# Kernel tuning notes

Measured on AMD Instinct MI355X. Metric: run time of the kernel, lower is better.

Reference implementation:

```python
import jax, jax.numpy as jnp
import numpy as np


def setup_inputs() -> dict:
    key = jax.random.key(0)
    k1, k2 = jax.random.split(key)
    N, M, D = 16384, 16384, 3
    target_pc = jax.random.normal(k1, (N, D), dtype=jnp.float32)
    output_pc = jax.random.normal(k2, (M, D), dtype=jnp.float32)
    return {"target_pc": target_pc, "output_pc": output_pc}


def _min_dist_sum(a, b):
    # sum over rows of min_j ||a_i - b_j||, via the norm-expansion trick
    sq_a = jnp.sum(a * a, axis=1, keepdims=True)          # [N,1]
    sq_b = jnp.sum(b * b, axis=1, keepdims=True).T        # [1,M]
    sq_dst = sq_a - 2.0 * (a @ b.T) + sq_b                # [N,M]
    dist = jnp.sqrt(jnp.maximum(sq_dst, 0.0))
    return jnp.sum(jnp.min(dist, axis=1))


def reference(target_pc, output_pc):
    loss_a_to_b = _min_dist_sum(output_pc, target_pc)
    loss_b_to_a = _min_dist_sum(target_pc, output_pc)
    return (loss_a_to_b + loss_b_to_a) / 1000.0
```

## Files before the change

### kernel.cpp

```cpp
#include <hip/hip_runtime.h>
#include <hip/hip_bf16.h>
#include <cfloat>

#define NPTS 16384
#define NTILES 512
#define R 2
#define BS 8
#define CPT (NTILES / BS)

typedef short short8  __attribute__((ext_vector_type(8)));
typedef float f32x16  __attribute__((ext_vector_type(16)));

__device__ inline short bf16s(float x) {
    __hip_bfloat16 h = __float2bfloat16(x);
    return *reinterpret_cast<short*>(&h);
}
__device__ inline float bf16f(short s) {
    __hip_bfloat16 h = *reinterpret_cast<__hip_bfloat16*>(&s);
    return __bfloat162float(h);
}

__global__ __launch_bounds__(256) void pack_kernel(
    const float* __restrict__ target, const float* __restrict__ output,
    short8* __restrict__ afrag, short8* __restrict__ bfrag,
    int* __restrict__ minsq, float* __restrict__ out)
{
    int t = blockIdx.x * 256 + threadIdx.x;
    if (t < 2 * NPTS) minsq[t] = 0x7F7F7F7F;
    if (t == 0) out[0] = 0.0f;

    int lane = t & 63;
    int tile = (t >> 6) & (NTILES - 1);
    int dir  = t >> 15;
    const float* __restrict__ A = dir ? target : output;
    const float* __restrict__ B = dir ? output : target;
    int p = tile * 32 + (lane & 31);
    int g = lane >> 5;
    int idx = (dir * NTILES + tile) * 64 + lane;

    {
        float x = A[3 * p], y = A[3 * p + 1], z = A[3 * p + 2];
        short hx = bf16s(x), hy = bf16s(y), hz = bf16s(z);
        short lx = bf16s(x - bf16f(hx)), ly = bf16s(y - bf16f(hy)), lz = bf16s(z - bf16f(hz));
        float sq = fmaf(x, x, fmaf(y, y, z * z));
        short sh = bf16s(sq), sl = bf16s(sq - bf16f(sh));
        const short one = 0x3F80;
        short8 loa = { hx, hy, hz, lx, ly, lz, hx, hy };
        short8 hia = { hz, one, one, sh, sl, 0, 0, 0 };
        afrag[idx] = g ? hia : loa;
    }
    {
        float x = B[3 * p], y = B[3 * p + 1], z = B[3 * p + 2];
        float nx = -2.f * x, ny = -2.f * y, nz = -2.f * z;
        short hx = bf16s(nx), hy = bf16s(ny), hz = bf16s(nz);
        short lx = bf16s(nx - bf16f(hx)), ly = bf16s(ny - bf16f(hy)), lz = bf16s(nz - bf16f(hz));
        float sq = fmaf(x, x, fmaf(y, y, z * z));
        short sh = bf16s(sq), sl = bf16s(sq - bf16f(sh));
        const short one = 0x3F80;
        short8 lob = { hx, hy, hz, hx, hy, hz, lx, ly };
        short8 hib = { lz, sh, sl, one, one, 0, 0, 0 };
        bfrag[idx] = g ? hib : lob;
    }
}

__global__ __launch_bounds__(256, 4) void chamfer_mfma_kernel(
    const short8* __restrict__ afrag, const short8* __restrict__ bfrag,
    int* __restrict__ minsq)
{
    const int lane = threadIdx.x & 63;
    const int wid  = blockIdx.x * 4 + (threadIdx.x >> 6);
    const int dir  = wid >> 11;
    const int rem  = wid & 2047;
    const int ag   = rem >> 3;
    const int bc   = rem & 7;

    const short8* __restrict__ af = afrag + (size_t)dir * NTILES * 64;
    const short8* __restrict__ gsrc = bfrag + (size_t)dir * NTILES * 64
                                            + (size_t)(bc * CPT) * 64;

    short8 a[R];
    #pragma unroll
    for (int r = 0; r < R; ++r)
        a[r] = af[(ag * R + r) * 64 + lane];

    f32x16 m[R];
    #pragma unroll
    for (int r = 0; r < R; ++r)
        m[r] = (f32x16)(FLT_MAX);

    const f32x16 zero = (f32x16)(0.0f);
    #pragma unroll 1
    for (int pp = 0; pp < CPT / 4; ++pp) {
        short8 b0 = gsrc[(4 * pp + 0) * 64 + lane];
        short8 b1 = gsrc[(4 * pp + 1) * 64 + lane];
        short8 b2 = gsrc[(4 * pp + 2) * 64 + lane];
        short8 b3 = gsrc[(4 * pp + 3) * 64 + lane];
        #pragma unroll
        for (int r = 0; r < R; ++r) {
            f32x16 c0 = __builtin_amdgcn_mfma_f32_32x32x16_bf16(a[r], b0, zero, 0, 0, 0);
            f32x16 c1 = __builtin_amdgcn_mfma_f32_32x32x16_bf16(a[r], b1, zero, 0, 0, 0);
            #pragma unroll
            for (int i = 0; i < 16; ++i)
                m[r][i] = fminf(m[r][i], fminf(c0[i], c1[i]));
            f32x16 c2 = __builtin_amdgcn_mfma_f32_32x32x16_bf16(a[r], b2, zero, 0, 0, 0);
            f32x16 c3 = __builtin_amdgcn_mfma_f32_32x32x16_bf16(a[r], b3, zero, 0, 0, 0);
            #pragma unroll
            for (int i = 0; i < 16; ++i)
                m[r][i] = fminf(m[r][i], fminf(c2[i], c3[i]));
        }
    }

    #pragma unroll
    for (int r = 0; r < R; ++r) {
        #pragma unroll
        for (int i = 0; i < 16; ++i) {
            float v = m[r][i];
            v = fminf(v, __shfl_xor(v, 1, 64));
            v = fminf(v, __shfl_xor(v, 2, 64));
            v = fminf(v, __shfl_xor(v, 4, 64));
            v = fminf(v, __shfl_xor(v, 8, 64));
            v = fminf(v, __shfl_xor(v, 16, 64));
            m[r][i] = v;
        }
    }

    if ((lane & 31) == 0) {
        const int g = lane >> 5;
        #pragma unroll
        for (int r = 0; r < R; ++r) {
            const int at = ag * R + r;
            #pragma unroll
            for (int i = 0; i < 16; ++i) {
                int row = (i & 3) + 8 * (i >> 2) + 4 * g;
                atomicMin(&minsq[dir * NPTS + at * 32 + row], __float_as_int(m[r][i]));
            }
        }
    }
}

__global__ __launch_bounds__(256) void reduce_kernel(
    const int* __restrict__ minsq, float* __restrict__ out)
{
    float s = 0.f;
    const int4* mv = (const int4*)minsq;
    for (int k = blockIdx.x * 256 + threadIdx.x; k < 2 * NPTS / 4; k += gridDim.x * 256) {
        int4 v = mv[k];
        s += sqrtf(fmaxf(__int_as_float(v.x), 0.f))
           + sqrtf(fmaxf(__int_as_float(v.y), 0.f))
           + sqrtf(fmaxf(__int_as_float(v.z), 0.f))
           + sqrtf(fmaxf(__int_as_float(v.w), 0.f));
    }
    for (int off = 32; off; off >>= 1) s += __shfl_down(s, off, 64);
    __shared__ float partial[4];
    if ((threadIdx.x & 63) == 0) partial[threadIdx.x >> 6] = s;
    __syncthreads();
    if (threadIdx.x == 0)
        atomicAdd(out, (partial[0] + partial[1] + partial[2] + partial[3]) * 0.001f);
}

extern "C" void kernel_launch(void* const* d_in, const int* in_sizes, int n_in,
                              void* d_out, int out_size, void* d_ws, size_t ws_size,
                              hipStream_t stream) {
    const float* target = (const float*)d_in[0];
    const float* output = (const float*)d_in[1];
    float* out = (float*)d_out;

    short8* afrag = (short8*)d_ws;
    short8* bfrag = afrag + 2 * NTILES * 64;
    int* minsq = (int*)(bfrag + 2 * NTILES * 64);

    pack_kernel<<<2 * NTILES * 64 / 256, 256, 0, stream>>>(
        target, output, afrag, bfrag, minsq, out);
    chamfer_mfma_kernel<<<1024, 256, 0, stream>>>(afrag, bfrag, minsq);
    reduce_kernel<<<32, 256, 0, stream>>>(minsq, out);
}
```

Measured before the change: 98.27 us.

## Switch chamfer distance MFMA from 32x32x16 to 16x16x32 tiles

Repacks both point fragments into 16-point tiles with a 32-wide K dimension, where the upper half of K is zero padding. The main kernel now issues 16x16x32 bf16 MFMAs, and each wave holds 8 A-tiles and sweeps 1/16 of the B tiles. The aim is smaller accumulators, a shorter cross-lane min reduction (one fewer shuffle stage) and more independent MFMAs per loaded B fragment. The cost is that each MFMA covers fewer point pairs and half of its K dimension is wasted, so total matrix-core cycles may rise.

New measurement: 104.6 us. 6.4% more time.

```diff
diff --git a/kernel.cpp b/kernel.cpp
--- a/kernel.cpp
+++ b/kernel.cpp
@@ -3,13 +3,13 @@
 #include <cfloat>
 
 #define NPTS 16384
-#define NTILES 512
-#define R 2
-#define BS 8
-#define CPT (NTILES / BS)
+#define NT16 1024
+#define R 8
+#define BS 16
+#define CPT (NT16 / BS)
 
 typedef short short8  __attribute__((ext_vector_type(8)));
-typedef float f32x16  __attribute__((ext_vector_type(16)));
+typedef float f32x4   __attribute__((ext_vector_type(4)));
 
 __device__ inline short bf16s(float x) {
     __hip_bfloat16 h = __float2bfloat16(x);
@@ -30,36 +30,39 @@
     if (t == 0) out[0] = 0.0f;
 
     int lane = t & 63;
-    int tile = (t >> 6) & (NTILES - 1);
-    int dir  = t >> 15;
+    int tile = (t >> 6) & (NT16 - 1);
+    int dir  = t >> 16;
     const float* __restrict__ A = dir ? target : output;
     const float* __restrict__ B = dir ? output : target;
-    int p = tile * 32 + (lane & 31);
-    int g = lane >> 5;
-    int idx = (dir * NTILES + tile) * 64 + lane;
+    int p = tile * 16 + (lane & 15);
+    int g = lane >> 4;
+    int idx = (dir * NT16 + tile) * 64 + lane;
+    const short one = 0x3F80;
+    short8 z = {0, 0, 0, 0, 0, 0, 0, 0};
 
     {
-        float x = A[3 * p], y = A[3 * p + 1], z = A[3 * p + 2];
-        short hx = bf16s(x), hy = bf16s(y), hz = bf16s(z);
-        short lx = bf16s(x - bf16f(hx)), ly = bf16s(y - bf16f(hy)), lz = bf16s(z - bf16f(hz));
-        float sq = fmaf(x, x, fmaf(y, y, z * z));
+        float x = A[3 * p], y = A[3 * p + 1], z3 = A[3 * p + 2];
+        short hx = bf16s(x), hy = bf16s(y), hz = bf16s(z3);
+        short lx = bf16s(x - bf16f(hx)), ly = bf16s(y - bf16f(hy)), lz = bf16s(z3 - bf16f(hz));
+        float sq = fmaf(x, x, fmaf(y, y, z3 * z3));
         short sh = bf16s(sq), sl = bf16s(sq - bf16f(sh));
-        const short one = 0x3F80;
-        short8 loa = { hx, hy, hz, lx, ly, lz, hx, hy };
-        short8 hia = { hz, one, one, sh, sl, 0, 0, 0 };
-        afrag[idx] = g ? hia : loa;
+        short8 g0 = { hx, hy, hz, lx, ly, lz, hx, hy };
+        short8 g1 = { hz, lx, ly, lz, sh, sl, one, one };
+        afrag[idx] = g == 0 ? g0 : (g == 1 ? g1 : z);
     }
     {
-        float x = B[3 * p], y = B[3 * p + 1], z = B[3 * p + 2];
-        float nx = -2.f * x, ny = -2.f * y, nz = -2.f * z;
+        float x = B[3 * p], y = B[3 * p + 1], z3 = B[3 * p + 2];
+        float nx = -2.f * x, ny = -2.f * y, nz = -2.f * z3;
         short hx = bf16s(nx), hy = bf16s(ny), hz = bf16s(nz);
         short lx = bf16s(nx - bf16f(hx)), ly = bf16s(ny - bf16f(hy)), lz = bf16s(nz - bf16f(hz));
-        float sq = fmaf(x, x, fmaf(y, y, z * z));
+        float sq = fmaf(x, x, fmaf(y, y, z3 * z3));
         short sh = bf16s(sq), sl = bf16s(sq - bf16f(sh));
-        const short one = 0x3F80;
-        short8 lob = { hx, hy, hz, hx, hy, hz, lx, ly };
-        short8 hib = { lz, sh, sl, one, one, 0, 0, 0 };
-        bfrag[idx] = g ? hib : lob;
+        short8 g0 = { hx, hy, hz, hx, hy, hz, lx, ly };
+        short8 g1 = { hz, lx, ly, lz, one, one, sh, sl };
+        short8 g1b = { hz , lx, ly, lz, one, one, sh, sl };
+        (void)g1; (void)g1b;
+        short8 bg1 = { lz, lx, ly, lz, one, one, sh, sl };
+        bfrag[idx] = g == 0 ? g0 : (g == 1 ? bg1 : z);
     }
 }
 
@@ -71,11 +74,11 @@
     const int wid  = blockIdx.x * 4 + (threadIdx.x >> 6);
     const int dir  = wid >> 11;
     const int rem  = wid & 2047;
-    const int ag   = rem >> 3;
-    const int bc   = rem & 7;
+    const int ag   = rem >> 4;
+    const int bc   = rem & 15;
 
-    const short8* __restrict__ af = afrag + (size_t)dir * NTILES * 64;
-    const short8* __restrict__ gsrc = bfrag + (size_t)dir * NTILES * 64
+    const short8* __restrict__ af = afrag + (size_t)dir * NT16 * 64;
+    const short8* __restrict__ gsrc = bfrag + (size_t)dir * NT16 * 64
                                             + (size_t)(bc * CPT) * 64;
 
     short8 a[R];
@@ -83,12 +86,12 @@
     for (int r = 0; r < R; ++r)
         a[r] = af[(ag * R + r) * 64 + lane];
 
-    f32x16 m[R];
+    f32x4 m[R];
     #pragma unroll
     for (int r = 0; r < R; ++r)
-        m[r] = (f32x16)(FLT_MAX);
+        m[r] = (f32x4)(FLT_MAX);
 
-    const f32x16 zero = (f32x16)(0.0f);
+    const f32x4 zero = (f32x4)(0.0f);
     #pragma unroll 1
     for (int pp = 0; pp < CPT / 4; ++pp) {
         short8 b0 = gsrc[(4 * pp + 0) * 64 + lane];
@@ -97,15 +100,15 @@
         short8 b3 = gsrc[(4 * pp + 3) * 64 + lane];
         #pragma unroll
         for (int r = 0; r < R; ++r) {
-            f32x16 c0 = __builtin_amdgcn_mfma_f32_32x32x16_bf16(a[r], b0, zero, 0, 0, 0);
-            f32x16 c1 = __builtin_amdgcn_mfma_f32_32x32x16_bf16(a[r], b1, zero, 0, 0, 0);
+            f32x4 c0 = __builtin_amdgcn_mfma_f32_16x16x32_bf16(a[r], b0, zero, 0, 0, 0);
+            f32x4 c1 = __builtin_amdgcn_mfma_f32_16x16x32_bf16(a[r], b1, zero, 0, 0, 0);
             #pragma unroll
-            for (int i = 0; i < 16; ++i)
+            for (int i = 0; i < 4; ++i)
                 m[r][i] = fminf(m[r][i], fminf(c0[i], c1[i]));
-            f32x16 c2 = __builtin_amdgcn_mfma_f32_32x32x16_bf16(a[r], b2, zero, 0, 0, 0);
-            f32x16 c3 = __builtin_amdgcn_mfma_f32_32x32x16_bf16(a[r], b3, zero, 0, 0, 0);
+            f32x4 c2 = __builtin_amdgcn_mfma_f32_16x16x32_bf16(a[r], b2, zero, 0, 0, 0);
+            f32x4 c3 = __builtin_amdgcn_mfma_f32_16x16x32_bf16(a[r], b3, zero, 0, 0, 0);
             #pragma unroll
-            for (int i = 0; i < 16; ++i)
+            for (int i = 0; i < 4; ++i)
                 m[r][i] = fminf(m[r][i], fminf(c2[i], c3[i]));
         }
     }
@@ -113,26 +116,25 @@
     #pragma unroll
     for (int r = 0; r < R; ++r) {
         #pragma unroll
-        for (int i = 0; i < 16; ++i) {
+        for (int i = 0; i < 4; ++i) {
             float v = m[r][i];
             v = fminf(v, __shfl_xor(v, 1, 64));
             v = fminf(v, __shfl_xor(v, 2, 64));
             v = fminf(v, __shfl_xor(v, 4, 64));
             v = fminf(v, __shfl_xor(v, 8, 64));
-            v = fminf(v, __shfl_xor(v, 16, 64));
             m[r][i] = v;
         }
     }
 
-    if ((lane & 31) == 0) {
-        const int g = lane >> 5;
+    if ((lane & 15) == 0) {
+        const int g = lane >> 4;
         #pragma unroll
         for (int r = 0; r < R; ++r) {
             const int at = ag * R + r;
             #pragma unroll
-            for (int i = 0; i < 16; ++i) {
-                int row = (i & 3) + 8 * (i >> 2) + 4 * g;
-                atomicMin(&minsq[dir * NPTS + at * 32 + row], __float_as_int(m[r][i]));
+            for (int i = 0; i < 4; ++i) {
+                int row = g * 4 + i;
+                atomicMin(&minsq[dir * NPTS + at * 16 + row], __float_as_int(m[r][i]));
             }
         }
     }
@@ -166,10 +168,10 @@
     float* out = (float*)d_out;
 
     short8* afrag = (short8*)d_ws;
-    short8* bfrag = afrag + 2 * NTILES * 64;
-    int* minsq = (int*)(bfrag + 2 * NTILES * 64);
+    short8* bfrag = afrag + 2 * NT16 * 64;
+    int* minsq = (int*)(bfrag + 2 * NT16 * 64);
 
-    pack_kernel<<<2 * NTILES * 64 / 256, 256, 0, stream>>>(
+    pack_kernel<<<2 * NT16 * 64 / 256, 256, 0, stream>>>(
         target, output, afrag, bfrag, minsq, out);
     chamfer_mfma_kernel<<<1024, 256, 0, stream>>>(afrag, bfrag, minsq);
     reduce_kernel<<<32, 256, 0, stream>>>(minsq, out);
```
